# Kernel tuning notes

Measured on AMD Instinct MI355X. Metric: run time of the kernel, lower is better.

The kernel has to match this reference:

```python
import jax, jax.numpy as jnp
import numpy as np

D = 512; N_HEAD = 8; D_HEAD = 64; D_INNER = 2048; SEG = 512; N_LAYER = 2; BATCH = 32
NUM_ITEMS = 50000
OMEGA = [2, 3, 4, 5, 7, 11, 21, 50]  # len == N_HEAD, required by multi-scale mask broadcast
EPS = 1e-8
STD = 0.02


def _layer_norm(x, w, b):
    mu = x.mean(-1, keepdims=True)
    var = ((x - mu) ** 2).mean(-1, keepdims=True)
    return (x - mu) / jnp.sqrt(var + EPS) * w + b


def _masks():
    # dir_mask: triu(ones, 1) (reverse=False); ms_mask[i,j,m] per omega band
    dir_mask = jnp.triu(jnp.ones((SEG, SEG), jnp.float32), 1)
    ms = np.stack([np.tri(SEG, SEG, o - 1) != np.tri(SEG, SEG, -o) for o in OMEGA], axis=-1)
    return dir_mask, jnp.asarray(ms)


def _pos_emb():
    freq = jnp.arange(0, D, 2, dtype=jnp.float32)
    inv_freq = 1.0 / jnp.power(10000.0, freq / D)
    pos_seq = jnp.arange(SEG, -SEG, -1.0, dtype=jnp.float32)  # length 2*SEG
    sinusoid = pos_seq[:, None] * inv_freq[None, :]
    return jnp.concatenate([jnp.sin(sinusoid), jnp.cos(sinusoid)], axis=-1)  # (2S, D)


def _rel_shift_bnij(x, klen):
    b, n, i, j2 = x.shape
    x = x.reshape(b, n, j2, i)[:, :, 1:, :].reshape(b, n, i, j2 - 1)
    return x[:, :, :, :klen]


def setup_inputs() -> dict:
    key = jax.random.key(0)
    ks = jax.random.split(key, 16)
    L = N_LAYER
    item_emb = STD * jax.random.normal(ks[0], (NUM_ITEMS + 1, D), jnp.float32)
    item_emb = item_emb.at[0].set(0.0)  # padding_idx=0
    proj = lambda k: STD * jax.random.normal(k, (L, D, N_HEAD, D_HEAD), jnp.float32)
    return {
        "input_ids": jax.random.randint(ks[1], (BATCH, SEG), 0, NUM_ITEMS + 1),
        "input_mask": jnp.zeros((BATCH, SEG), jnp.float32),
        "item_emb": item_emb,
        "Wq": proj(ks[2]), "Wk": proj(ks[3]), "Wv": proj(ks[4]),
        "Wr": proj(ks[5]), "Wo": proj(ks[6]),
        "r_r_bias": STD * jax.random.normal(ks[7], (L, N_HEAD, D_HEAD), jnp.float32),
        "r_w_bias": STD * jax.random.normal(ks[8], (L, N_HEAD, D_HEAD), jnp.float32),
        "ln_attn_w": jnp.ones((L, D), jnp.float32), "ln_attn_b": jnp.zeros((L, D), jnp.float32),
        "W1": STD * jax.random.normal(ks[9], (L, D, D_INNER), jnp.float32),
        "b1": jnp.zeros((L, D_INNER), jnp.float32),
        "W2": STD * jax.random.normal(ks[10], (L, D_INNER, D), jnp.float32),
        "b2": jnp.zeros((L, D), jnp.float32),
        "ln_ff_w": jnp.ones((L, D), jnp.float32), "ln_ff_b": jnp.zeros((L, D), jnp.float32),
    }


def reference(input_ids, input_mask, item_emb, Wq, Wk, Wv, Wr, Wo, r_r_bias, r_w_bias,
              ln_attn_w, ln_attn_b, W1, b1, W2, b2, ln_ff_w, ln_ff_b):
    ids = input_ids.T                      # (S, B)
    im = input_mask.T.astype(jnp.float32)  # (S, B)
    dir_mask, ms_mask = _masks()
    # data_mask: (q,k,b); attn_mask: (q,k,b,n) via multi-scale bands (training path)
    data_mask = im[None, :, :] + im[:, None, :] + dir_mask[:, :, None]
    attn_mask = ((data_mask[:, :, :, None] + (~ms_mask)[:, :, None, :].astype(jnp.float32)) > 0).astype(jnp.float32)
    mask_bnij = jnp.transpose(attn_mask, (2, 3, 0, 1))  # (b,n,i,j)

    h = item_emb[ids]          # (S, B, D)
    pos = _pos_emb()           # (2S, D), shared across batch
    scale = 1.0 / np.sqrt(D_HEAD).astype(np.float32)

    for l in range(N_LAYER):
        k_h = jnp.einsum('ibh,hnd->ibnd', h, Wk[l])
        v_h = jnp.einsum('ibh,hnd->ibnd', h, Wv[l])
        k_r = jnp.einsum('jh,hnd->jnd', pos, Wr[l])   # pos shared across batch
        q_h = jnp.einsum('ibh,hnd->ibnd', h, Wq[l])
        ac = jnp.einsum('ibnd,jbnd->bnij', q_h + r_w_bias[l], k_h)
        bd = jnp.einsum('ibnd,jnd->bnij', q_h + r_r_bias[l], k_r)
        bd = _rel_shift_bnij(bd, SEG)
        attn_score = (ac + bd) * scale - 1e30 * mask_bnij
        attn_prob = jax.nn.softmax(attn_score, axis=3)
        attn_vec = jnp.einsum('bnij,jbnd->ibnd', attn_prob, v_h)
        attn_out = jnp.einsum('ibnd,hnd->ibh', attn_vec, Wo[l])
        h = _layer_norm(attn_out + h, ln_attn_w[l], ln_attn_b[l])
        ff = jax.nn.gelu(h @ W1[l] + b1[l], approximate=False) @ W2[l] + b2[l]
        h = _layer_norm(ff + h, ln_ff_w[l], ln_ff_b[l])

    return jnp.transpose(h, (1, 0, 2))  # (B, S, D)
```

## Files before the change

### kernel.cpp

```cpp
#include <hip/hip_runtime.h>
#include <math.h>


#define S_  512
#define B_  32
#define D_  512
#define NH  8
#define DH  64
#define DI  2048
#define M_  (S_*B_)
#define QKV_LD 1536
#define WL  3407872
#define FP32_ONE 0x3F800000u

typedef unsigned short ushort_t;
typedef __attribute__((ext_vector_type(8))) short short8;
typedef __attribute__((ext_vector_type(4))) float f32x4;

__constant__ int OMEGA_C[8] = {2, 3, 4, 5, 7, 11, 21, 50};

__device__ __forceinline__ float b2f(ushort_t us) {
    return __uint_as_float(((unsigned int)us) << 16);
}
__device__ __forceinline__ ushort_t f2b(float f) {
    unsigned int u = __float_as_uint(f);
    return (ushort_t)((u + 0x7fffu + ((u >> 16) & 1u)) >> 16);
}
__device__ __forceinline__ float ldx(const void* p, size_t idx, bool isbf) {
    return isbf ? b2f(((const ushort_t*)p)[idx]) : ((const float*)p)[idx];
}
__device__ __forceinline__ void async16(const ushort_t* g, ushort_t* l) {
    __builtin_amdgcn_global_load_lds(
        (const __attribute__((address_space(1))) unsigned int*)g,
        (__attribute__((address_space(3))) unsigned int*)l, 16, 0, 0);
}

#define DPPA(v, ctrl) v += __int_as_float(__builtin_amdgcn_update_dpp(0, __float_as_int(v), ctrl, 0xf, 0xf, true))
__device__ __forceinline__ void dpp_sum64(float& v) {
    DPPA(v, 0x111); DPPA(v, 0x112); DPPA(v, 0x114);
    DPPA(v, 0x118); DPPA(v, 0x142); DPPA(v, 0x143);
}
#define DPPROR(v, ctrl) __int_as_float(__builtin_amdgcn_update_dpp(__float_as_int(v), __float_as_int(v), ctrl, 0xf, 0xf, false))
__device__ __forceinline__ float row16_sum(float v) {
    v += DPPROR(v, 0x128); v += DPPROR(v, 0x124);
    v += DPPROR(v, 0x122); v += DPPROR(v, 0x121);
    return v;
}
__device__ __forceinline__ float row16_max(float v) {
    v = fmaxf(v, DPPROR(v, 0x128)); v = fmaxf(v, DPPROR(v, 0x124));
    v = fmaxf(v, DPPROR(v, 0x122)); v = fmaxf(v, DPPROR(v, 0x121));
    return v;
}
__device__ __forceinline__ float rlane(float v, int l) {
    return __int_as_float(__builtin_amdgcn_readlane(__float_as_int(v), l));
}

__global__ __launch_bounds__(256) void embed_kernel(const int* __restrict__ ids,
                                                    const void* __restrict__ emb,
                                                    ushort_t* __restrict__ h,
                                                    const unsigned int* __restrict__ dtp) {
    const bool isbf = (dtp[0] != FP32_ONE);
    int idx = blockIdx.x * 256 + threadIdx.x;
    int d8 = idx & 63;
    int row = idx >> 6;
    int s = row >> 5, b = row & 31;
    int id = ids[b * S_ + s];
    size_t src = (size_t)id * D_ + d8 * 8;
    if (isbf) {
        *(uint4*)(h + (size_t)row * D_ + d8 * 8) = *(const uint4*)((const ushort_t*)emb + src);
    } else {
        const float* e = (const float*)emb + src;
        float4 a0 = ((const float4*)e)[0], a1 = ((const float4*)e)[1];
        uint4 pk;
        pk.x = (unsigned)f2b(a0.x) | ((unsigned)f2b(a0.y) << 16);
        pk.y = (unsigned)f2b(a0.z) | ((unsigned)f2b(a0.w) << 16);
        pk.z = (unsigned)f2b(a1.x) | ((unsigned)f2b(a1.y) << 16);
        pk.w = (unsigned)f2b(a1.z) | ((unsigned)f2b(a1.w) << 16);
        *(uint4*)(h + (size_t)row * D_ + d8 * 8) = pk;
    }
}

__global__ __launch_bounds__(256) void posemb_kernel(ushort_t* __restrict__ pos) {
    int flat = blockIdx.x * 256 + threadIdx.x;
    int p = flat >> 8, k = flat & 255;
    float inv = expf((float)k * -0.035977892078031f);
    float val = (512.0f - (float)p) * inv;
    pos[p * D_ + k]       = f2b(sinf(val));
    pos[p * D_ + 256 + k] = f2b(cosf(val));
}

__global__ __launch_bounds__(256) void transp_cvt4(
    const void* __restrict__ s0, const void* __restrict__ s1,
    const void* __restrict__ s2, const void* __restrict__ s3,
    ushort_t* __restrict__ wbuf, const unsigned int* __restrict__ dtp) {
    const bool isbf = (dtp[0] != FP32_ONE);
    __shared__ float tt[32][33];
    int z = blockIdx.z, layer = z >> 2, t4 = z & 3;
    const void* srcs[4] = {s0, s1, s2, s3};
    const void* in = srcs[t4];
    size_t inoff = (size_t)layer * 262144;
    ushort_t* out = wbuf + (size_t)layer * WL + (size_t)t4 * 262144;
    int tx = threadIdx.x & 31, ty = threadIdx.x >> 5;
    int n0 = blockIdx.x * 32, k0 = blockIdx.y * 32;
#pragma unroll
    for (int it = 0; it < 4; ++it)
        tt[ty + it * 8][tx] = ldx(in, inoff + (size_t)(k0 + ty + it * 8) * 512 + n0 + tx, isbf);
    __syncthreads();
#pragma unroll
    for (int it = 0; it < 4; ++it)
        out[(size_t)(n0 + ty + it * 8) * 512 + k0 + tx] = f2b(tt[tx][ty + it * 8]);
}

__global__ __launch_bounds__(256) void transp_cvtL(const void* __restrict__ in, size_t perlin,
                                                   ushort_t* __restrict__ wbuf, size_t outoff,
                                                   const unsigned int* __restrict__ dtp,
                                                   int K, int N) {
    const bool isbf = (dtp[0] != FP32_ONE);
    __shared__ float tt[32][33];
    int layer = blockIdx.z;
    size_t inoff = (size_t)layer * perlin;
    ushort_t* out = wbuf + (size_t)layer * WL + outoff;
    int tx = threadIdx.x & 31, ty = threadIdx.x >> 5;
    int n0 = blockIdx.x * 32, k0 = blockIdx.y * 32;
#pragma unroll
    for (int it = 0; it < 4; ++it)
        tt[ty + it * 8][tx] = ldx(in, inoff + (size_t)(k0 + ty + it * 8) * N + n0 + tx, isbf);
    __syncthreads();
#pragma unroll
    for (int it = 0; it < 4; ++it)
        out[(size_t)(n0 + ty + it * 8) * K + k0 + tx] = f2b(tt[tx][ty + it * 8]);
}

__global__ __launch_bounds__(256) void cvtL(const void* __restrict__ in, size_t perlin,
                                            ushort_t* __restrict__ wbuf, size_t outoff,
                                            const unsigned int* __restrict__ dtp, int nelem) {
    const bool isbf = (dtp[0] != FP32_ONE);
    int layer = blockIdx.z;
    int i = blockIdx.x * 256 + threadIdx.x;
    if (i < nelem)
        wbuf[(size_t)layer * WL + outoff + i] = f2b(ldx(in, (size_t)layer * perlin + i, isbf));
}

template<int EPI, int OUT>
__global__ __launch_bounds__(256)
void mfma_gemm(const ushort_t* __restrict__ A, int lda,
               const ushort_t* __restrict__ Bt, int ldb,
               const void* __restrict__ biasv, size_t biasoff,
               void* __restrict__ Cv, int ldc,
               const unsigned int* __restrict__ dtp, int M, int N, int K) {
    const bool isbf = (dtp[0] != FP32_ONE);
    __shared__ ushort_t As[128 * 32];
    __shared__ ushort_t Bs[128 * 32];
    const int tid = threadIdx.x;
    const int bm = blockIdx.x * 128, bn = blockIdx.y * 128;
    const int w = tid >> 6, lane = tid & 63;
    const int wr = w >> 1, wc = w & 1;
    const int quad = lane >> 4, l16 = lane & 15;
    const int rsub = lane >> 2;
    const int kcg  = (lane & 3) ^ ((rsub >> 1) & 3);
    const int fsw  = (l16 >> 1) & 3;

    f32x4 acc[4][4];
#pragma unroll
    for (int i = 0; i < 4; ++i)
#pragma unroll
        for (int j = 0; j < 4; ++j)
#pragma unroll
            for (int r = 0; r < 4; ++r) acc[i][j][r] = 0.f;

    for (int k0 = 0; k0 < K; k0 += 32) {
#pragma unroll
        for (int c = 0; c < 2; ++c) {
            int grp = c * 4 + w;
            int row = grp * 16 + rsub;
            async16(A  + (size_t)(bm + row) * lda + k0 + kcg * 8, As + grp * 512);
            async16(Bt + (size_t)(bn + row) * ldb + k0 + kcg * 8, Bs + grp * 512);
        }
        __syncthreads();

        short8 af[4], bf[4];
#pragma unroll
        for (int t = 0; t < 4; ++t) {
            int ra = wr * 64 + t * 16 + l16;
            int rb = wc * 64 + t * 16 + l16;
            af[t] = *(const short8*)(As + ra * 32 + ((quad ^ fsw) * 8));
            bf[t] = *(const short8*)(Bs + rb * 32 + ((quad ^ fsw) * 8));
        }
#pragma unroll
        for (int tr = 0; tr < 4; ++tr)
#pragma unroll
            for (int tc = 0; tc < 4; ++tc)
                acc[tr][tc] = __builtin_amdgcn_mfma_f32_16x16x32_bf16(bf[tc], af[tr], acc[tr][tc], 0, 0, 0);
        __syncthreads();
    }

    float bv[4][4];
    if (EPI >= 1) {
#pragma unroll
        for (int tc = 0; tc < 4; ++tc)
#pragma unroll
            for (int r = 0; r < 4; ++r)
                bv[tc][r] = ldx(biasv, biasoff + bn + wc * 64 + tc * 16 + quad * 4 + r, isbf);
    }
#pragma unroll
    for (int tr = 0; tr < 4; ++tr) {
        int grow = bm + wr * 64 + tr * 16 + l16;
#pragma unroll
        for (int tc = 0; tc < 4; ++tc) {
            int gcb = bn + wc * 64 + tc * 16 + quad * 4;
            float x[4];
#pragma unroll
            for (int r = 0; r < 4; ++r) {
                float v = acc[tr][tc][r];
                if (EPI >= 1) v += bv[tc][r];
                if (EPI == 2) v = 0.5f * v * (1.f + erff(v * 0.7071067811865475f));
                x[r] = v;
            }
            size_t coff = (size_t)grow * ldc + gcb;
            if (OUT == 0) {
                uint2 pk;
                pk.x = (unsigned)f2b(x[0]) | ((unsigned)f2b(x[1]) << 16);
                pk.y = (unsigned)f2b(x[2]) | ((unsigned)f2b(x[3]) << 16);
                *(uint2*)((ushort_t*)Cv + coff) = pk;
            } else if (OUT == 1) {
                *(float4*)((float*)Cv + coff) = make_float4(x[0], x[1], x[2], x[3]);
            } else {
                float4* p = (float4*)((float*)Cv + coff);
                float4 o = *p;
                o.x += x[0]; o.y += x[1]; o.z += x[2]; o.w += x[3];
                *p = o;
            }
        }
    }
}

__global__ __launch_bounds__(256) void attn_mfma(
    ushort_t* __restrict__ qkv, const ushort_t* __restrict__ krb,
    const void* __restrict__ rwb, const void* __restrict__ rrb, size_t boff,
    const void* __restrict__ im,
    const unsigned int* __restrict__ dtp) {
    const bool isbf = (dtp[0] != FP32_ONE);
    __shared__ ushort_t Ks[128 * 64];
    __shared__ ushort_t VT[64 * 128];
    __shared__ ushort_t Rs[64 * 64];
    __shared__ float    BD2[4 * 16 * 64];
    __shared__ ushort_t Ps[4 * 16 * 128];
    __shared__ float    imk[128];
    __shared__ float    imq[64];

    const int tid = threadIdx.x;
    const int i0 = blockIdx.x * 64;
    const int b  = blockIdx.y;
    const int n  = blockIdx.z;
    const int o  = OMEGA_C[n];
    const int noff = n * DH;
    const int j0 = i0 - 64;
    const int w = tid >> 6, lane = tid & 63;
    const int quad = lane >> 4, l16 = lane & 15;

#pragma unroll
    for (int it = 0; it < 4; ++it) {
        int q4 = it * 256 + tid;
        int c  = q4 >> 3, ch = q4 & 7;
        int jc = j0 + c; jc = jc < 0 ? 0 : jc;
        size_t rowb = (size_t)(jc * B_ + b) * QKV_LD + noff;
        *(uint4*)(Ks + c * 64 + ch * 8) = *(const uint4*)(qkv + rowb + 512 + ch * 8);
        ushort_t v8[8];
        *(uint4*)v8 = *(const uint4*)(qkv + rowb + 1024 + ch * 8);
#pragma unroll
        for (int e = 0; e < 8; ++e) VT[(ch * 8 + e) * 128 + c] = v8[e];
    }
#pragma unroll
    for (int it = 0; it < 2; ++it) {
        int q4 = it * 256 + tid;
        int m = q4 >> 3, ch = q4 & 7;
        *(uint4*)(Rs + m * 64 + ch * 8) =
            *(const uint4*)(krb + (size_t)(512 - m) * 512 + noff + ch * 8);
    }
    if (tid < 128) {
        int j = j0 + tid;
        imk[tid] = (j >= 0) ? ldx(im, b * S_ + j, isbf) : 0.f;
    } else if (tid < 192) {
        imq[tid - 128] = ldx(im, b * S_ + i0 + (tid - 128), isbf);
    }
    __syncthreads();

    const int qrow = i0 + w * 16 + l16;
    size_t qbase = (size_t)(qrow * B_ + b) * QKV_LD + noff;
    short8 aw[2], ar[2];
#pragma unroll
    for (int kc = 0; kc < 2; ++kc) {
        int kof = kc * 32 + quad * 8;
        ushort_t qe[8];
        *(uint4*)qe = *(const uint4*)(qkv + qbase + kof);
#pragma unroll
        for (int e = 0; e < 8; ++e) {
            float f = b2f(qe[e]);
            ((ushort_t*)&aw[kc])[e] = f2b(f + ldx(rwb, boff + noff + kof + e, isbf));
            ((ushort_t*)&ar[kc])[e] = f2b(f + ldx(rrb, boff + noff + kof + e, isbf));
        }
    }

    f32x4 accs[8];
#pragma unroll
    for (int ct = 0; ct < 8; ++ct) {
        short8 b0 = *(const short8*)(Ks + (ct * 16 + l16) * 64 + quad * 8);
        short8 b1 = *(const short8*)(Ks + (ct * 16 + l16) * 64 + 32 + quad * 8);
        f32x4 z = {0.f, 0.f, 0.f, 0.f};
        z = __builtin_amdgcn_mfma_f32_16x16x32_bf16(aw[0], b0, z, 0, 0, 0);
        z = __builtin_amdgcn_mfma_f32_16x16x32_bf16(aw[1], b1, z, 0, 0, 0);
        accs[ct] = z;
    }
    float* BD2w = BD2 + w * 16 * 64;
#pragma unroll
    for (int mt = 0; mt < 4; ++mt) {
        short8 b0 = *(const short8*)(Rs + (mt * 16 + l16) * 64 + quad * 8);
        short8 b1 = *(const short8*)(Rs + (mt * 16 + l16) * 64 + 32 + quad * 8);
        f32x4 z = {0.f, 0.f, 0.f, 0.f};
        z = __builtin_amdgcn_mfma_f32_16x16x32_bf16(ar[0], b0, z, 0, 0, 0);
        z = __builtin_amdgcn_mfma_f32_16x16x32_bf16(ar[1], b1, z, 0, 0, 0);
#pragma unroll
        for (int r = 0; r < 4; ++r)
            BD2w[(quad * 4 + r) * 64 + mt * 16 + l16] = z[r];
    }

    float im_i[4];
#pragma unroll
    for (int r = 0; r < 4; ++r) im_i[r] = imq[w * 16 + quad * 4 + r];

    float sc[8][4];
#pragma unroll
    for (int ct = 0; ct < 8; ++ct) {
        int cl = ct * 16 + l16;
        float imk_c = imk[cl];
#pragma unroll
        for (int r = 0; r < 4; ++r) {
            int qrl = w * 16 + quad * 4 + r;
            int rel = qrl + 64 - cl;
            int relc = rel < 0 ? 0 : (rel > 63 ? 63 : rel);
            float bd = BD2w[(quad * 4 + r) * 64 + relc];
            bool valid = (rel >= 0) && (rel < o) && (rel <= i0 + qrl)
                         && (im_i[r] + imk_c <= 0.f);
            sc[ct][r] = valid ? (accs[ct][r] + bd) * 0.125f : -1e30f;
        }
    }
    float rl[4];
#pragma unroll
    for (int r = 0; r < 4; ++r) {
        float mx = sc[0][r];
#pragma unroll
        for (int ct = 1; ct < 8; ++ct) mx = fmaxf(mx, sc[ct][r]);
        mx = row16_max(mx);
        float l = 0.f;
#pragma unroll
        for (int ct = 0; ct < 8; ++ct) {
            float pv = expf(sc[ct][r] - mx);
            sc[ct][r] = pv;
            l += pv;
        }
        l = row16_sum(l);
        rl[r] = 1.f / l;
    }
    ushort_t* Pw = Ps + w * 16 * 128;
#pragma unroll
    for (int ct = 0; ct < 8; ++ct)
#pragma unroll
        for (int r = 0; r < 4; ++r)
            Pw[(quad * 4 + r) * 128 + ct * 16 + l16] = f2b(sc[ct][r] * rl[r]);

    short8 aP[4];
#pragma unroll
    for (int kc = 0; kc < 4; ++kc)
        aP[kc] = *(const short8*)(Pw + l16 * 128 + kc * 32 + quad * 8);

    const int qg = i0 + w * 16 + l16;
    const size_t obase = (size_t)(qg * B_ + b) * QKV_LD + noff;
#pragma unroll
    for (int dt = 0; dt < 4; ++dt) {
        f32x4 accO = {0.f, 0.f, 0.f, 0.f};
#pragma unroll
        for (int kc = 0; kc < 4; ++kc) {
            short8 bV = *(const short8*)(VT + (dt * 16 + l16) * 128 + kc * 32 + quad * 8);
            accO = __builtin_amdgcn_mfma_f32_16x16x32_bf16(aP[kc], bV, accO, 0, 0, 0);
        }
        f32x4 accT = {0.f, 0.f, 0.f, 0.f};
#pragma unroll
        for (int kc = 0; kc < 4; ++kc) {
            short8 bV = *(const short8*)(VT + (dt * 16 + l16) * 128 + kc * 32 + quad * 8);
            accT = __builtin_amdgcn_mfma_f32_16x16x32_bf16(bV, aP[kc], accT, 0, 0, 0);
        }
        (void)accO;
        uint2 pk;
        pk.x = (unsigned)f2b(accT[0]) | ((unsigned)f2b(accT[1]) << 16);
        pk.y = (unsigned)f2b(accT[2]) | ((unsigned)f2b(accT[3]) << 16);
        *(uint2*)(qkv + obase + dt * 16 + quad * 4) = pk;
    }
}

template<int XF>
__global__ __launch_bounds__(256) void add_ln_kernel(
    const void* __restrict__ x, ushort_t* __restrict__ h,
    const void* __restrict__ w, const void* __restrict__ b, size_t boff,
    const unsigned int* __restrict__ dtp) {
    const bool isbf = (dtp[0] != FP32_ONE);
    int lane = threadIdx.x & 63;
    int row = blockIdx.x * 4 + (threadIdx.x >> 6);
    size_t base = (size_t)row * D_ + lane * 8;
    float v[8];
    if (XF) {
        const float* xp = (const float*)x + base;
        float4 a0 = ((const float4*)xp)[0], a1 = ((const float4*)xp)[1];
        v[0] = a0.x; v[1] = a0.y; v[2] = a0.z; v[3] = a0.w;
        v[4] = a1.x; v[5] = a1.y; v[6] = a1.z; v[7] = a1.w;
    } else {
        ushort_t xe[8];
        *(uint4*)xe = *(const uint4*)((const ushort_t*)x + base);
#pragma unroll
        for (int e = 0; e < 8; ++e) v[e] = b2f(xe[e]);
    }
    ushort_t he[8];
    *(uint4*)he = *(const uint4*)(h + base);
    float s = 0.f, ss = 0.f;
#pragma unroll
    for (int e = 0; e < 8; ++e) {
        v[e] += b2f(he[e]);
        s += v[e]; ss += v[e] * v[e];
    }
    dpp_sum64(s); dpp_sum64(ss);
    float S = rlane(s, 63), SS = rlane(ss, 63);
    float mu  = S * (1.f / D_);
    float var = fmaxf(SS * (1.f / D_) - mu * mu, 0.f);
    float inv = rsqrtf(var + 1e-8f);
    ushort_t oe[8];
#pragma unroll
    for (int e = 0; e < 8; ++e)
        oe[e] = f2b((v[e] - mu) * inv * ldx(w, boff + lane * 8 + e, isbf)
                    + ldx(b, boff + lane * 8 + e, isbf));
    *(uint4*)(h + base) = *(uint4*)oe;
}

__global__ __launch_bounds__(256) void writeout_kernel(const ushort_t* __restrict__ h,
                                                       void* __restrict__ out,
                                                       const unsigned int* __restrict__ dtp) {
    const bool isbf = (dtp[0] != FP32_ONE);
    int idx = blockIdx.x * 256 + threadIdx.x;
    int d8 = idx & 63;
    int rest = idx >> 6;
    int s = rest & (S_ - 1), b = rest >> 9;
    ushort_t ve[8];
    *(uint4*)ve = *(const uint4*)(h + ((size_t)(s * B_ + b) << 9) + d8 * 8);
    if (isbf) {
        *(uint4*)((ushort_t*)out + (size_t)idx * 8) = *(uint4*)ve;
    } else {
        float* op = (float*)out + (size_t)idx * 8;
        ((float4*)op)[0] = make_float4(b2f(ve[0]), b2f(ve[1]), b2f(ve[2]), b2f(ve[3]));
        ((float4*)op)[1] = make_float4(b2f(ve[4]), b2f(ve[5]), b2f(ve[6]), b2f(ve[7]));
    }
}

extern "C" void kernel_launch(void* const* d_in, const int* in_sizes, int n_in,
                              void* d_out, int out_size, void* d_ws, size_t ws_size,
                              hipStream_t stream) {
    (void)in_sizes; (void)n_in; (void)out_size; (void)ws_size;
    const int*  ids = (const int*)d_in[0];
    const void* im  = d_in[1];
    const void* emb = d_in[2];
    const void* Wq = d_in[3], *Wk = d_in[4], *Wv = d_in[5], *Wr = d_in[6], *Wo = d_in[7];
    const void* rrb = d_in[8], *rwb = d_in[9];
    const void* lnaw = d_in[10], *lnab = d_in[11];
    const void* W1 = d_in[12], *b1 = d_in[13], *W2 = d_in[14], *b2 = d_in[15];
    const void* lnfw = d_in[16], *lnfb = d_in[17];
    const unsigned int* dtp = (const unsigned int*)d_in[10];

    char* wsb = (char*)d_ws;
    ushort_t* h     = (ushort_t*)wsb;
    ushort_t* qkv   = (ushort_t*)(wsb + (16u << 20));
    ushort_t* ff1c  = (ushort_t*)(wsb + (16u << 20));
    float*    acc32 = (float*)   (wsb + (48u << 20));
    ushort_t* tmp   = (ushort_t*)(wsb + (64u << 20));
    ushort_t* wbuf  = (ushort_t*)(wsb + (80u << 20));
    ushort_t* posb  = (ushort_t*)(wsb + (93u << 20));
    ushort_t* krb   = (ushort_t*)(wsb + (94u << 20));

    embed_kernel<<<4096, 256, 0, stream>>>(ids, emb, h, dtp);
    posemb_kernel<<<1024, 256, 0, stream>>>(posb);

    transp_cvt4<<<dim3(16, 16, 8), 256, 0, stream>>>(Wq, Wk, Wv, Wr, wbuf, dtp);
    cvtL<<<dim3(1024, 1, 2), 256, 0, stream>>>(Wo, 262144, wbuf, 1048576, dtp, 262144);
    transp_cvtL<<<dim3(64, 16, 2), 256, 0, stream>>>(W1, 1048576, wbuf, 1310720, dtp, 512, 2048);
    transp_cvtL<<<dim3(16, 64, 2), 256, 0, stream>>>(W2, 1048576, wbuf, 2359296, dtp, 2048, 512);

    for (int l = 0; l < 2; ++l) {
        size_t boff = (size_t)l * 512;
        size_t b1off = (size_t)l * 2048;
        ushort_t* qkvT = wbuf + (size_t)l * WL;
        ushort_t* wrT  = qkvT + 786432;
        ushort_t* woc  = wrT  + 262144;
        ushort_t* w1T  = woc  + 262144;
        ushort_t* w2T  = w1T  + 1048576;

        mfma_gemm<0,0><<<dim3(8, 4), 256, 0, stream>>>(posb, 512, wrT, 512, nullptr, 0, krb, 512, dtp, 1024, 512, 512);
        mfma_gemm<0,0><<<dim3(128, 12), 256, 0, stream>>>(h, 512, qkvT, 512, nullptr, 0, qkv, QKV_LD, dtp, M_, QKV_LD, 512);

        attn_mfma<<<dim3(8, 32, 8), 256, 0, stream>>>(qkv, krb, rwb, rrb, boff, im, dtp);

        mfma_gemm<0,0><<<dim3(128, 4), 256, 0, stream>>>(qkv, QKV_LD, woc, 512, nullptr, 0, tmp, 512, dtp, M_, 512, 512);
        add_ln_kernel<0><<<4096, 256, 0, stream>>>(tmp, h, lnaw, lnab, boff, dtp);

        for (int nh = 0; nh < 2; ++nh) {
            ushort_t* w1part = w1T + (size_t)nh * 1024 * 512;
            ushort_t* w2part = w2T + (size_t)nh * 1024;
            mfma_gemm<2,0><<<dim3(128, 8), 256, 0, stream>>>(h, 512, w1part, 512, b1, b1off + nh * 1024, ff1c, 1024, dtp, M_, 1024, 512);
            if (nh == 0)
                mfma_gemm<1,1><<<dim3(128, 4), 256, 0, stream>>>(ff1c, 1024, w2part, 2048, b2, boff, acc32, 512, dtp, M_, 512, 1024);
            else
                mfma_gemm<0,2><<<dim3(128, 4), 256, 0, stream>>>(ff1c, 1024, w2part, 2048, nullptr, 0, acc32, 512, dtp, M_, 512, 1024);
        }
        add_ln_kernel<1><<<4096, 256, 0, stream>>>(acc32, h, lnfw, lnfb, boff, dtp);
    }

    writeout_kernel<<<4096, 256, 0, stream>>>(h, d_out, dtp);
}
```

Measured before the change: 869.3 us.

## Run FFN as single full-width GEMMs with bf16 output, drop dead MFMA

The FFN no longer splits into two halves. It now runs one W1 GEMM over the full 2048 inner dimension into a larger bf16 buffer, then one W2 GEMM with K=2048 that writes bf16 directly. This removes the fp32 accumulation buffer and its read-modify-write pass. The unused accO MFMA loop in attention is deleted, and both layers' positional key projections are hoisted before the loop. The trade-offs are a larger workspace and rounding the FFN output to bf16 before the residual layer norm.

```diff
diff --git a/kernel.cpp b/kernel.cpp
--- a/kernel.cpp
+++ b/kernel.cpp
@@ -141,12 +141,12 @@
         wbuf[(size_t)layer * WL + outoff + i] = f2b(ldx(in, (size_t)layer * perlin + i, isbf));
 }
 
-template<int EPI, int OUT>
+template<int EPI>
 __global__ __launch_bounds__(256)
 void mfma_gemm(const ushort_t* __restrict__ A, int lda,
                const ushort_t* __restrict__ Bt, int ldb,
                const void* __restrict__ biasv, size_t biasoff,
-               void* __restrict__ Cv, int ldc,
+               ushort_t* __restrict__ C, int ldc,
                const unsigned int* __restrict__ dtp, int M, int N, int K) {
     const bool isbf = (dtp[0] != FP32_ONE);
     __shared__ ushort_t As[128 * 32];
@@ -216,20 +216,10 @@
                 if (EPI == 2) v = 0.5f * v * (1.f + erff(v * 0.7071067811865475f));
                 x[r] = v;
             }
-            size_t coff = (size_t)grow * ldc + gcb;
-            if (OUT == 0) {
-                uint2 pk;
-                pk.x = (unsigned)f2b(x[0]) | ((unsigned)f2b(x[1]) << 16);
-                pk.y = (unsigned)f2b(x[2]) | ((unsigned)f2b(x[3]) << 16);
-                *(uint2*)((ushort_t*)Cv + coff) = pk;
-            } else if (OUT == 1) {
-                *(float4*)((float*)Cv + coff) = make_float4(x[0], x[1], x[2], x[3]);
-            } else {
-                float4* p = (float4*)((float*)Cv + coff);
-                float4 o = *p;
-                o.x += x[0]; o.y += x[1]; o.z += x[2]; o.w += x[3];
-                *p = o;
-            }
+            uint2 pk;
+            pk.x = (unsigned)f2b(x[0]) | ((unsigned)f2b(x[1]) << 16);
+            pk.y = (unsigned)f2b(x[2]) | ((unsigned)f2b(x[3]) << 16);
+            *(uint2*)(C + (size_t)grow * ldc + gcb) = pk;
         }
     }
 }
@@ -377,19 +367,12 @@
     const size_t obase = (size_t)(qg * B_ + b) * QKV_LD + noff;
 #pragma unroll
     for (int dt = 0; dt < 4; ++dt) {
-        f32x4 accO = {0.f, 0.f, 0.f, 0.f};
-#pragma unroll
-        for (int kc = 0; kc < 4; ++kc) {
-            short8 bV = *(const short8*)(VT + (dt * 16 + l16) * 128 + kc * 32 + quad * 8);
-            accO = __builtin_amdgcn_mfma_f32_16x16x32_bf16(aP[kc], bV, accO, 0, 0, 0);
-        }
         f32x4 accT = {0.f, 0.f, 0.f, 0.f};
 #pragma unroll
         for (int kc = 0; kc < 4; ++kc) {
             short8 bV = *(const short8*)(VT + (dt * 16 + l16) * 128 + kc * 32 + quad * 8);
             accT = __builtin_amdgcn_mfma_f32_16x16x32_bf16(bV, aP[kc], accT, 0, 0, 0);
         }
-        (void)accO;
         uint2 pk;
         pk.x = (unsigned)f2b(accT[0]) | ((unsigned)f2b(accT[1]) << 16);
         pk.y = (unsigned)f2b(accT[2]) | ((unsigned)f2b(accT[3]) << 16);
@@ -397,33 +380,22 @@
     }
 }
 
-template<int XF>
 __global__ __launch_bounds__(256) void add_ln_kernel(
-    const void* __restrict__ x, ushort_t* __restrict__ h,
+    const ushort_t* __restrict__ x, ushort_t* __restrict__ h,
     const void* __restrict__ w, const void* __restrict__ b, size_t boff,
     const unsigned int* __restrict__ dtp) {
     const bool isbf = (dtp[0] != FP32_ONE);
     int lane = threadIdx.x & 63;
     int row = blockIdx.x * 4 + (threadIdx.x >> 6);
     size_t base = (size_t)row * D_ + lane * 8;
+    ushort_t xe[8], he[8];
+    *(uint4*)xe = *(const uint4*)(x + base);
+    *(uint4*)he = *(const uint4*)(h + base);
     float v[8];
-    if (XF) {
-        const float* xp = (const float*)x + base;
-        float4 a0 = ((const float4*)xp)[0], a1 = ((const float4*)xp)[1];
-        v[0] = a0.x; v[1] = a0.y; v[2] = a0.z; v[3] = a0.w;
-        v[4] = a1.x; v[5] = a1.y; v[6] = a1.z; v[7] = a1.w;
-    } else {
-        ushort_t xe[8];
-        *(uint4*)xe = *(const uint4*)((const ushort_t*)x + base);
-#pragma unroll
-        for (int e = 0; e < 8; ++e) v[e] = b2f(xe[e]);
-    }
-    ushort_t he[8];
-    *(uint4*)he = *(const uint4*)(h + base);
     float s = 0.f, ss = 0.f;
 #pragma unroll
     for (int e = 0; e < 8; ++e) {
-        v[e] += b2f(he[e]);
+        v[e] = b2f(xe[e]) + b2f(he[e]);
         s += v[e]; ss += v[e] * v[e];
     }
     dpp_sum64(s); dpp_sum64(ss);
@@ -473,14 +445,14 @@
     const unsigned int* dtp = (const unsigned int*)d_in[10];
 
     char* wsb = (char*)d_ws;
-    ushort_t* h     = (ushort_t*)wsb;
-    ushort_t* qkv   = (ushort_t*)(wsb + (16u << 20));
-    ushort_t* ff1c  = (ushort_t*)(wsb + (16u << 20));
-    float*    acc32 = (float*)   (wsb + (48u << 20));
-    ushort_t* tmp   = (ushort_t*)(wsb + (64u << 20));
-    ushort_t* wbuf  = (ushort_t*)(wsb + (80u << 20));
-    ushort_t* posb  = (ushort_t*)(wsb + (93u << 20));
-    ushort_t* krb   = (ushort_t*)(wsb + (94u << 20));
+    ushort_t* h    = (ushort_t*)wsb;
+    ushort_t* qkv  = (ushort_t*)(wsb + (16u << 20));
+    ushort_t* tmp  = (ushort_t*)(wsb + (64u << 20));
+    ushort_t* ff1  = (ushort_t*)(wsb + (80u << 20));
+    ushort_t* wbuf = (ushort_t*)(wsb + (144u << 20));
+    ushort_t* posb = (ushort_t*)(wsb + (157u << 20));
+    ushort_t* krb0 = (ushort_t*)(wsb + (158u << 20));
+    ushort_t* krb1 = (ushort_t*)(wsb + (159u << 20));
 
     embed_kernel<<<4096, 256, 0, stream>>>(ids, emb, h, dtp);
     posemb_kernel<<<1024, 256, 0, stream>>>(posb);
@@ -490,33 +462,28 @@
     transp_cvtL<<<dim3(64, 16, 2), 256, 0, stream>>>(W1, 1048576, wbuf, 1310720, dtp, 512, 2048);
     transp_cvtL<<<dim3(16, 64, 2), 256, 0, stream>>>(W2, 1048576, wbuf, 2359296, dtp, 2048, 512);
 
+    mfma_gemm<0><<<dim3(8, 4), 256, 0, stream>>>(posb, 512, wbuf + 786432, 512, nullptr, 0, krb0, 512, dtp, 1024, 512, 512);
+    mfma_gemm<0><<<dim3(8, 4), 256, 0, stream>>>(posb, 512, wbuf + WL + 786432, 512, nullptr, 0, krb1, 512, dtp, 1024, 512, 512);
+
     for (int l = 0; l < 2; ++l) {
         size_t boff = (size_t)l * 512;
         size_t b1off = (size_t)l * 2048;
         ushort_t* qkvT = wbuf + (size_t)l * WL;
-        ushort_t* wrT  = qkvT + 786432;
-        ushort_t* woc  = wrT  + 262144;
+        ushort_t* woc  = qkvT + 1048576;
         ushort_t* w1T  = woc  + 262144;
         ushort_t* w2T  = w1T  + 1048576;
-
-        mfma_gemm<0,0><<<dim3(8, 4), 256, 0, stream>>>(posb, 512, wrT, 512, nullptr, 0, krb, 512, dtp, 1024, 512, 512);
-        mfma_gemm<0,0><<<dim3(128, 12), 256, 0, stream>>>(h, 512, qkvT, 512, nullptr, 0, qkv, QKV_LD, dtp, M_, QKV_LD, 512);
+        ushort_t* krb  = l ? krb1 : krb0;
+
+        mfma_gemm<0><<<dim3(128, 12), 256, 0, stream>>>(h, 512, qkvT, 512, nullptr, 0, qkv, QKV_LD, dtp, M_, QKV_LD, 512);
 
         attn_mfma<<<dim3(8, 32, 8), 256, 0, stream>>>(qkv, krb, rwb, rrb, boff, im, dtp);
 
-        mfma_gemm<0,0><<<dim3(128, 4), 256, 0, stream>>>(qkv, QKV_LD, woc, 512, nullptr, 0, tmp, 512, dtp, M_, 512, 512);
-        add_ln_kernel<0><<<4096, 256, 0, stream>>>(tmp, h, lnaw, lnab, boff, dtp);
-
-        for (int nh = 0; nh < 2; ++nh) {
-            ushort_t* w1part = w1T + (size_t)nh * 1024 * 512;
-            ushort_t* w2part = w2T + (size_t)nh * 1024;
-            mfma_gemm<2,0><<<dim3(128, 8), 256, 0, stream>>>(h, 512, w1part, 512, b1, b1off + nh * 1024, ff1c, 1024, dtp, M_, 1024, 512);
-            if (nh == 0)
-                mfma_gemm<1,1><<<dim3(128, 4), 256, 0, stream>>>(ff1c, 1024, w2part, 2048, b2, boff, acc32, 512, dtp, M_, 512, 1024);
-            else
-                mfma_gemm<0,2><<<dim3(128, 4), 256, 0, stream>>>(ff1c, 1024, w2part, 2048, nullptr, 0, acc32, 512, dtp, M_, 512, 1024);
-        }
-        add_ln_kernel<1><<<4096, 256, 0, stream>>>(acc32, h, lnfw, lnfb, boff, dtp);
+        mfma_gemm<0><<<dim3(128, 4), 256, 0, stream>>>(qkv, QKV_LD, woc, 512, nullptr, 0, tmp, 512, dtp, M_, 512, 512);
+        add_ln_kernel<<<4096, 256, 0, stream>>>(tmp, h, lnaw, lnab, boff, dtp);
+
+        mfma_gemm<2><<<dim3(128, 16), 256, 0, stream>>>(h, 512, w1T, 512, b1, b1off, ff1, DI, dtp, M_, DI, 512);
+        mfma_gemm<1><<<dim3(128, 4),  256, 0, stream>>>(ff1, DI, w2T, 2048, b2, boff, tmp, 512, dtp, M_, 512, DI);
+        add_ln_kernel<<<4096, 256, 0, stream>>>(tmp, h, lnfw, lnfb, boff, dtp);
     }
 
     writeout_kernel<<<4096, 256, 0, stream>>>(h, d_out, dtp);
```

After: 811.6 us. 6.6% less time.
